# Kernel tuning notes

Measured on AMD Instinct MI355X. Metric: run time of the kernel, lower is better.

The kernel has to match this reference:

```python
import jax, jax.numpy as jnp
import numpy as np
from jax import lax

KSIZE = 7
EPS = 1e-10


def _circular_mask(k=KSIZE):
    # faithful to EdgeLoss.cal_mask: inclusive circle, normalized by count
    xs = np.arange(k, dtype=np.float32)
    d2 = (xs[:, None] + 0.5 - k / 2) ** 2 + (xs[None, :] + 0.5 - k / 2) ** 2
    m = (d2 <= ((k - 1) / 2) ** 2).astype(np.float32)
    return jnp.asarray(m / m.sum())


def _gather_logp(prob, target):
    # prob: (B,C,H,W), target: (B,H,W) int -> log prob at target class, (B,1,H,W)
    logpt = jnp.log(prob + EPS)
    return jnp.take_along_axis(logpt, target[:, None, :, :], axis=1)


def _focal0(prob, target):
    # FocalLoss(gamma=0, alpha=None): mean of -log p_t
    return jnp.mean(-_gather_logp(prob, target))


def _dice(prob, target):
    t = target.astype(prob.dtype)          # (B,H,W)
    p = prob[:, 1, :, :]                   # foreground channel
    I = jnp.sum(p * t, axis=(1, 2))
    U = jnp.sum(p + t, axis=(1, 2))
    return 1.0 - jnp.mean(2.0 * I / (U + EPS))


def _edge(prob, target, mask):
    # circular box-filter average of target == unfold+mask sum (zero padding)
    t = target.astype(prob.dtype)[:, None, :, :]  # (B,1,H,W)
    ave = lax.conv_general_dilated(t, mask[None, None, :, :], (1, 1), 'SAME')
    at = jnp.abs(t - ave)                          # edge weight (B,1,H,W)
    lp = _gather_logp(prob, target)                # (B,1,H,W)
    return jnp.mean(-lp * at)


def _calloss(prob, target, sigmas, mask):
    return (_focal0(prob, target) / sigmas[0]
            + _dice(prob, target) / sigmas[1]
            + _edge(prob, target, mask) / sigmas[2])


def setup_inputs() -> dict:
    key = jax.random.key(0)
    k1, k2, k3, k4, k5 = jax.random.split(key, 5)
    N, M, B, C, H, W = 2, 1, 8, 2, 1024, 1024
    predictions = jax.random.normal(k1, (N, B, C, H, W), dtype=jnp.float32)
    Diss = jax.random.uniform(k2, (M, B, C, H, W), dtype=jnp.float32)
    target = jax.random.randint(k3, (B, H, W), 0, 2, dtype=jnp.int32)
    diff = jax.random.normal(k4, (), dtype=jnp.float32)
    sigma = jax.random.uniform(k5, (3,), dtype=jnp.float32, minval=0.5, maxval=1.5)
    return {"predictions": predictions, "Diss": Diss, "target": target,
            "diff": diff, "sigma": sigma}


def reference(predictions, Diss, target, diff, sigma):
    mask = _circular_mask()
    sigmas = sigma * sigma
    loss = jnp.asarray(0.0, dtype=predictions.dtype)
    for i in range(predictions.shape[0]):            # deep-supervision heads
        prob = jax.nn.softmax(predictions[i], axis=1)
        loss = loss + _calloss(prob, target, sigmas, mask)
    for j in range(Diss.shape[0]):                   # already-probabilities
        loss = loss + _calloss(Diss[j], target, sigmas, mask)
    loss = loss + diff                               # len(diff) != 0 branch
    loss = loss + jnp.sum(jnp.log(sigmas)) / 2
    return loss
```

## Files before the change

### kernel.cpp

```cpp
#include <hip/hip_runtime.h>
#include <math.h>

#define BB 8
#define HH 1024
#define WW 1024
#define HW (1024*1024)

#define TW 128
#define TH 16
#define HALO_H (TH+6)
#define TSTRIDE 136
#define NCOPY 32
#define NSLOT 18

__global__ __launch_bounds__(256, 8)
void loss_main(const float* __restrict__ pred,
               const float* __restrict__ diss,
               const int*   __restrict__ target,
               double*      __restrict__ acc)
{
    __shared__ __align__(16) unsigned char tile[HALO_H][TSTRIDE];
    __shared__ __align__(16) unsigned char h5[HALO_H][TW];
    __shared__ __align__(16) unsigned char h7[HALO_H][TW];
    __shared__ float red[4][12];

    const int bx = blockIdx.x;
    const int by = blockIdx.y;
    const int b  = blockIdx.z;
    const int x0 = bx * TW, y0 = by * TH;
    const int tid = threadIdx.x;
    const int txx = tid & 31;
    const int ty  = tid >> 5;

    const int* tgt_b = target + (size_t)b * HW;
    for (int ch = tid; ch < HALO_H * 34; ch += 256) {
        int r = ch / 34;
        int m = ch - r * 34;
        int gy  = y0 - 3 + r;
        int gxb = x0 - 4 + 4 * m;
        unsigned v = 0u;
        if (gy >= 0 && gy < HH) {
            if (gxb >= 0 && gxb + 3 < WW) {
                const int4 iv = *(const int4*)(tgt_b + (size_t)gy * WW + gxb);
                v = (unsigned)(iv.x & 0xff)
                  | ((unsigned)(iv.y & 0xff) << 8)
                  | ((unsigned)(iv.z & 0xff) << 16)
                  | ((unsigned)(iv.w & 0xff) << 24);
            } else {
                #pragma unroll
                for (int j = 0; j < 4; ++j) {
                    int gx = gxb + j;
                    if (gx >= 0 && gx < WW)
                        v |= (unsigned)(tgt_b[(size_t)gy * WW + gx] & 0xff) << (8 * j);
                }
            }
        }
        *(unsigned*)&tile[r][4 * m] = v;
    }
    __syncthreads();

    for (int g = tid; g < HALO_H * 32; g += 256) {
        int r  = g >> 5;
        int xg = (g & 31) << 2;
        unsigned c0 = *(const unsigned*)&tile[r][xg];
        unsigned c1 = *(const unsigned*)&tile[r][xg + 4];
        unsigned c2 = *(const unsigned*)&tile[r][xg + 8];
        unsigned A1 = (c0 >> 8)  | (c1 << 24);
        unsigned A2 = (c0 >> 16) | (c1 << 16);
        unsigned A3 = (c0 >> 24) | (c1 << 8);
        unsigned A5 = (c1 >> 8)  | (c2 << 24);
        unsigned A6 = (c1 >> 16) | (c2 << 16);
        unsigned A7 = (c1 >> 24) | (c2 << 8);
        unsigned v5 = A2 + A3 + c1 + A5 + A6;
        unsigned v7 = v5 + A1 + A7;
        *(unsigned*)&h5[r][xg] = v5;
        *(unsigned*)&h7[r][xg] = v7;
    }
    __syncthreads();

    const float* p00 = pred + ((size_t)(0 * BB + b) * 2 + 0) * HW;
    const float* p01 = p00 + HW;
    const float* p10 = pred + ((size_t)(1 * BB + b) * 2 + 0) * HW;
    const float* p11 = p10 + HW;
    const float* q0  = diss + ((size_t)b * 2 + 0) * HW;
    const float* q1  = q0 + HW;

    float sf0=0.f, se0=0.f, si0=0.f, su0=0.f;
    float sf1=0.f, se1=0.f, si1=0.f, su1=0.f;
    float sf2=0.f, se2=0.f, si2=0.f, su2=0.f;

    const int x  = txx * 4;
    const int gx = x0 + x;
    #pragma unroll
    for (int k = 0; k < 2; ++k) {
        const int r  = ty + 8 * k;
        const int gy = y0 + r;
        const size_t off = (size_t)gy * WW + gx;

        const unsigned t4   = *(const unsigned*)&tile[r + 3][x + 4];
        const unsigned cnt4 = *(const unsigned*)&tile[r    ][x + 4]
                            + *(const unsigned*)&tile[r + 6][x + 4]
                            + *(const unsigned*)&h5[r + 1][x]
                            + *(const unsigned*)&h5[r + 2][x]
                            + *(const unsigned*)&h7[r + 3][x]
                            + *(const unsigned*)&h5[r + 4][x]
                            + *(const unsigned*)&h5[r + 5][x];

        float4 v00 = *(const float4*)(p00 + off);
        float4 v01 = *(const float4*)(p01 + off);
        float4 v10 = *(const float4*)(p10 + off);
        float4 v11 = *(const float4*)(p11 + off);
        float4 w0  = *(const float4*)(q0  + off);
        float4 w1  = *(const float4*)(q1  + off);

        #pragma unroll
        for (int j = 0; j < 4; ++j) {
            const unsigned tb = (t4 >> (8 * j)) & 0xffu;
            const float t  = (float)tb;
            const float at = fabsf(t - (float)((cnt4 >> (8 * j)) & 0xffu) * (1.0f / 29.0f));
            {
                float a0 = ((const float*)&v00)[j], a1 = ((const float*)&v01)[j];
                float p1v = __builtin_amdgcn_rcpf(1.0f + __expf(a0 - a1));
                float pt  = (tb != 0u) ? p1v : 1.0f - p1v;
                float lp  = __logf(pt + 1e-10f);
                sf0 -= lp; se0 -= lp * at; si0 += p1v * t; su0 += p1v + t;
            }
            {
                float a0 = ((const float*)&v10)[j], a1 = ((const float*)&v11)[j];
                float p1v = __builtin_amdgcn_rcpf(1.0f + __expf(a0 - a1));
                float pt  = (tb != 0u) ? p1v : 1.0f - p1v;
                float lp  = __logf(pt + 1e-10f);
                sf1 -= lp; se1 -= lp * at; si1 += p1v * t; su1 += p1v + t;
            }
            {
                float d0 = ((const float*)&w0)[j], d1 = ((const float*)&w1)[j];
                float pt = (tb != 0u) ? d1 : d0;
                float lp = __logf(pt + 1e-10f);
                sf2 -= lp; se2 -= lp * at; si2 += d1 * t; su2 += d1 + t;
            }
        }
    }

    float vals[12] = {sf0,se0,si0,su0, sf1,se1,si1,su1, sf2,se2,si2,su2};
    #pragma unroll
    for (int j = 0; j < 12; ++j) {
        float v = vals[j];
        #pragma unroll
        for (int s = 32; s > 0; s >>= 1) v += __shfl_down(v, s, 64);
        vals[j] = v;
    }
    const int wave = tid >> 6;
    const int lane = tid & 63;
    if (lane == 0) {
        #pragma unroll
        for (int j = 0; j < 12; ++j) red[wave][j] = vals[j];
    }
    __syncthreads();
    if (tid < 12) {
        double s = (double)red[0][tid] + (double)red[1][tid]
                 + (double)red[2][tid] + (double)red[3][tid];
        const int img  = tid >> 2;
        const int what = tid & 3;
        int slot;
        if      (what == 0) slot = 0;
        else if (what == 1) slot = 1;
        else if (what == 2) slot = 2 + b;
        else                slot = 10 + b;
        const int copy = (by * 8 + bx) & (NCOPY - 1);
        unsafeAtomicAdd(acc + ((size_t)(img * NSLOT + slot) * NCOPY + copy), s);
    }
}

__global__ __launch_bounds__(256)
void finalize_kernel(const double* __restrict__ acc,
                     const float*  __restrict__ diff,
                     const float*  __restrict__ sigma,
                     float*        __restrict__ out)
{
    __shared__ double ssum[54];
    const int t = threadIdx.x;
    if (t < 216) {
        const int slot_lin = t >> 2;
        const int part     = t & 3;
        const double* p = acc + (size_t)slot_lin * NCOPY + part * 8;
        double s = 0.0;
        #pragma unroll
        for (int j = 0; j < 8; ++j) s += p[j];
        s += __shfl_down(s, 1, 64);
        s += __shfl_down(s, 2, 64);
        if (part == 0) ssum[slot_lin] = s;
    }
    __syncthreads();
    if (t == 0) {
        const double sig0 = (double)sigma[0] * (double)sigma[0];
        const double sig1 = (double)sigma[1] * (double)sigma[1];
        const double sig2 = (double)sigma[2] * (double)sigma[2];
        const double inv  = 1.0 / (double)((size_t)BB * HW);
        double loss = 0.0;
        for (int i = 0; i < 3; ++i) {
            const double* A = ssum + i * NSLOT;
            double focal = A[0] * inv;
            double edge  = A[1] * inv;
            double dsum  = 0.0;
            for (int b = 0; b < BB; ++b)
                dsum += 2.0 * A[2 + b] / (A[10 + b] + 1e-10);
            double dice = 1.0 - dsum / (double)BB;
            loss += focal / sig0 + dice / sig1 + edge / sig2;
        }
        loss += (double)diff[0];
        loss += 0.5 * (log(sig0) + log(sig1) + log(sig2));
        out[0] = (float)loss;
    }
}

extern "C" void kernel_launch(void* const* d_in, const int* in_sizes, int n_in,
                              void* d_out, int out_size, void* d_ws, size_t ws_size,
                              hipStream_t stream)
{
    const float* pred   = (const float*)d_in[0];
    const float* diss   = (const float*)d_in[1];
    const int*   target = (const int*)  d_in[2];
    const float* diff   = (const float*)d_in[3];
    const float* sigma  = (const float*)d_in[4];
    double* acc = (double*)d_ws;

    hipMemsetAsync(d_ws, 0, (size_t)3 * NSLOT * NCOPY * sizeof(double), stream);

    dim3 grid(WW / TW, HH / TH, BB);
    loss_main<<<grid, 256, 0, stream>>>(pred, diss, target, acc);
    finalize_kernel<<<1, 256, 0, stream>>>(acc, diff, sigma, (float*)d_out);
}
```

Before: 271.4 us.

## Prefetch prediction loads before target staging and spread atomic accumulator copies

Issues all twelve float4 global loads of predictions and Diss before the target tile is staged into LDS and the box sums are built, so that memory latency overlaps the halo construction and barriers. It hoists the LDS neighbourhood-count reads, accumulates the target sum once instead of once per image, and lowers the occupancy hint to 6 to make room for the extra live registers. It also doubles the number of accumulator copies and changes their layout to copy-major with a stride of 64, which spreads atomic contention across more addresses. The cost is higher register pressure and lower occupancy.

After: 272.0 us. No clear change (+0.2%).

```diff
diff --git a/kernel.cpp b/kernel.cpp
--- a/kernel.cpp
+++ b/kernel.cpp
@@ -10,10 +10,11 @@
 #define TH 16
 #define HALO_H (TH+6)
 #define TSTRIDE 136
-#define NCOPY 32
+#define NCOPY 64
+#define CSTRIDE 64
 #define NSLOT 18
 
-__global__ __launch_bounds__(256, 8)
+__global__ __launch_bounds__(256, 6)
 void loss_main(const float* __restrict__ pred,
                const float* __restrict__ diss,
                const int*   __restrict__ target,
@@ -31,6 +32,31 @@
     const int tid = threadIdx.x;
     const int txx = tid & 31;
     const int ty  = tid >> 5;
+
+    const float* p00 = pred + ((size_t)(0 * BB + b) * 2 + 0) * HW;
+    const float* p01 = p00 + HW;
+    const float* p10 = pred + ((size_t)(1 * BB + b) * 2 + 0) * HW;
+    const float* p11 = p10 + HW;
+    const float* q0  = diss + ((size_t)b * 2 + 0) * HW;
+    const float* q1  = q0 + HW;
+
+    const int x  = txx * 4;
+    const int gx = x0 + x;
+    const size_t offA = (size_t)(y0 + ty) * WW + gx;
+    const size_t offB = offA + (size_t)8 * WW;
+
+    const float4 v00a = *(const float4*)(p00 + offA);
+    const float4 v01a = *(const float4*)(p01 + offA);
+    const float4 v10a = *(const float4*)(p10 + offA);
+    const float4 v11a = *(const float4*)(p11 + offA);
+    const float4 w0a  = *(const float4*)(q0  + offA);
+    const float4 w1a  = *(const float4*)(q1  + offA);
+    const float4 v00b = *(const float4*)(p00 + offB);
+    const float4 v01b = *(const float4*)(p01 + offB);
+    const float4 v10b = *(const float4*)(p10 + offB);
+    const float4 v11b = *(const float4*)(p11 + offB);
+    const float4 w0b  = *(const float4*)(q0  + offB);
+    const float4 w1b  = *(const float4*)(q1  + offB);
 
     const int* tgt_b = target + (size_t)b * HW;
     for (int ch = tid; ch < HALO_H * 34; ch += 256) {
@@ -49,9 +75,9 @@
             } else {
                 #pragma unroll
                 for (int j = 0; j < 4; ++j) {
-                    int gx = gxb + j;
-                    if (gx >= 0 && gx < WW)
-                        v |= (unsigned)(tgt_b[(size_t)gy * WW + gx] & 0xff) << (8 * j);
+                    int gxj = gxb + j;
+                    if (gxj >= 0 && gxj < WW)
+                        v |= (unsigned)(tgt_b[(size_t)gy * WW + gxj] & 0xff) << (8 * j);
                 }
             }
         }
@@ -78,70 +104,69 @@
     }
     __syncthreads();
 
-    const float* p00 = pred + ((size_t)(0 * BB + b) * 2 + 0) * HW;
-    const float* p01 = p00 + HW;
-    const float* p10 = pred + ((size_t)(1 * BB + b) * 2 + 0) * HW;
-    const float* p11 = p10 + HW;
-    const float* q0  = diss + ((size_t)b * 2 + 0) * HW;
-    const float* q1  = q0 + HW;
-
-    float sf0=0.f, se0=0.f, si0=0.f, su0=0.f;
-    float sf1=0.f, se1=0.f, si1=0.f, su1=0.f;
-    float sf2=0.f, se2=0.f, si2=0.f, su2=0.f;
-
-    const int x  = txx * 4;
-    const int gx = x0 + x;
+    float sf0=0.f, se0=0.f, si0=0.f, sp0=0.f;
+    float sf1=0.f, se1=0.f, si1=0.f, sp1=0.f;
+    float sf2=0.f, se2=0.f, si2=0.f, sd1=0.f;
+    float st = 0.f;
+
+    const unsigned t4a   = *(const unsigned*)&tile[ty + 3][x + 4];
+    const unsigned cnt4a = *(const unsigned*)&tile[ty    ][x + 4]
+                         + *(const unsigned*)&tile[ty + 6][x + 4]
+                         + *(const unsigned*)&h5[ty + 1][x]
+                         + *(const unsigned*)&h5[ty + 2][x]
+                         + *(const unsigned*)&h7[ty + 3][x]
+                         + *(const unsigned*)&h5[ty + 4][x]
+                         + *(const unsigned*)&h5[ty + 5][x];
+    const unsigned t4b   = *(const unsigned*)&tile[ty + 11][x + 4];
+    const unsigned cnt4b = *(const unsigned*)&tile[ty +  8][x + 4]
+                         + *(const unsigned*)&tile[ty + 14][x + 4]
+                         + *(const unsigned*)&h5[ty +  9][x]
+                         + *(const unsigned*)&h5[ty + 10][x]
+                         + *(const unsigned*)&h7[ty + 11][x]
+                         + *(const unsigned*)&h5[ty + 12][x]
+                         + *(const unsigned*)&h5[ty + 13][x];
+
     #pragma unroll
     for (int k = 0; k < 2; ++k) {
-        const int r  = ty + 8 * k;
-        const int gy = y0 + r;
-        const size_t off = (size_t)gy * WW + gx;
-
-        const unsigned t4   = *(const unsigned*)&tile[r + 3][x + 4];
-        const unsigned cnt4 = *(const unsigned*)&tile[r    ][x + 4]
-                            + *(const unsigned*)&tile[r + 6][x + 4]
-                            + *(const unsigned*)&h5[r + 1][x]
-                            + *(const unsigned*)&h5[r + 2][x]
-                            + *(const unsigned*)&h7[r + 3][x]
-                            + *(const unsigned*)&h5[r + 4][x]
-                            + *(const unsigned*)&h5[r + 5][x];
-
-        float4 v00 = *(const float4*)(p00 + off);
-        float4 v01 = *(const float4*)(p01 + off);
-        float4 v10 = *(const float4*)(p10 + off);
-        float4 v11 = *(const float4*)(p11 + off);
-        float4 w0  = *(const float4*)(q0  + off);
-        float4 w1  = *(const float4*)(q1  + off);
+        const unsigned t4   = k ? t4b   : t4a;
+        const unsigned cnt4 = k ? cnt4b : cnt4a;
+        const float4&  v00  = k ? v00b : v00a;
+        const float4&  v01  = k ? v01b : v01a;
+        const float4&  v10  = k ? v10b : v10a;
+        const float4&  v11  = k ? v11b : v11a;
+        const float4&  w0   = k ? w0b  : w0a;
+        const float4&  w1   = k ? w1b  : w1a;
 
         #pragma unroll
         for (int j = 0; j < 4; ++j) {
             const unsigned tb = (t4 >> (8 * j)) & 0xffu;
             const float t  = (float)tb;
             const float at = fabsf(t - (float)((cnt4 >> (8 * j)) & 0xffu) * (1.0f / 29.0f));
+            st += t;
             {
                 float a0 = ((const float*)&v00)[j], a1 = ((const float*)&v01)[j];
                 float p1v = __builtin_amdgcn_rcpf(1.0f + __expf(a0 - a1));
                 float pt  = (tb != 0u) ? p1v : 1.0f - p1v;
                 float lp  = __logf(pt + 1e-10f);
-                sf0 -= lp; se0 -= lp * at; si0 += p1v * t; su0 += p1v + t;
+                sf0 -= lp; se0 -= lp * at; si0 += p1v * t; sp0 += p1v;
             }
             {
                 float a0 = ((const float*)&v10)[j], a1 = ((const float*)&v11)[j];
                 float p1v = __builtin_amdgcn_rcpf(1.0f + __expf(a0 - a1));
                 float pt  = (tb != 0u) ? p1v : 1.0f - p1v;
                 float lp  = __logf(pt + 1e-10f);
-                sf1 -= lp; se1 -= lp * at; si1 += p1v * t; su1 += p1v + t;
+                sf1 -= lp; se1 -= lp * at; si1 += p1v * t; sp1 += p1v;
             }
             {
                 float d0 = ((const float*)&w0)[j], d1 = ((const float*)&w1)[j];
                 float pt = (tb != 0u) ? d1 : d0;
                 float lp = __logf(pt + 1e-10f);
-                sf2 -= lp; se2 -= lp * at; si2 += d1 * t; su2 += d1 + t;
+                sf2 -= lp; se2 -= lp * at; si2 += d1 * t; sd1 += d1;
             }
         }
     }
 
-    float vals[12] = {sf0,se0,si0,su0, sf1,se1,si1,su1, sf2,se2,si2,su2};
+    float vals[12] = {sf0,se0,si0,sp0+st, sf1,se1,si1,sp1+st, sf2,se2,si2,sd1+st};
     #pragma unroll
     for (int j = 0; j < 12; ++j) {
         float v = vals[j];
@@ -167,7 +192,7 @@
         else if (what == 2) slot = 2 + b;
         else                slot = 10 + b;
         const int copy = (by * 8 + bx) & (NCOPY - 1);
-        unsafeAtomicAdd(acc + ((size_t)(img * NSLOT + slot) * NCOPY + copy), s);
+        unsafeAtomicAdd(acc + (size_t)copy * CSTRIDE + (img * NSLOT + slot), s);
     }
 }
 
@@ -182,10 +207,10 @@
     if (t < 216) {
         const int slot_lin = t >> 2;
         const int part     = t & 3;
-        const double* p = acc + (size_t)slot_lin * NCOPY + part * 8;
+        const double* p = acc + slot_lin + (size_t)part * 16 * CSTRIDE;
         double s = 0.0;
         #pragma unroll
-        for (int j = 0; j < 8; ++j) s += p[j];
+        for (int j = 0; j < 16; ++j) s += p[(size_t)j * CSTRIDE];
         s += __shfl_down(s, 1, 64);
         s += __shfl_down(s, 2, 64);
         if (part == 0) ssum[slot_lin] = s;
@@ -224,7 +249,7 @@
     const float* sigma  = (const float*)d_in[4];
     double* acc = (double*)d_ws;
 
-    hipMemsetAsync(d_ws, 0, (size_t)3 * NSLOT * NCOPY * sizeof(double), stream);
+    hipMemsetAsync(d_ws, 0, (size_t)NCOPY * CSTRIDE * sizeof(double), stream);
 
     dim3 grid(WW / TW, HH / TH, BB);
     loss_main<<<grid, 256, 0, stream>>>(pred, diss, target, acc);
```

## Pipeline per-block row slabs with async global-to-LDS double buffering

Applied to the files above, without the earlier changes.

Each block now covers a 128x128 region and walks it in 8-row slabs. Prediction and Diss rows are staged into double-buffered LDS with async global_load_lds, and the next target tile and its horizontal sums are prepared while the current slab is computed. This hides memory latency inside each block rather than relying on many short-lived blocks. It also counts target sums once per block instead of per image, and spreads the atomic accumulators over more copies with a transposed layout. The cost is a larger LDS footprint, fewer resident blocks, and more barriers.

Result: slower. 277.8 us (+2.3%).

```diff
diff --git a/kernel.cpp b/kernel.cpp
--- a/kernel.cpp
+++ b/kernel.cpp
@@ -8,157 +8,253 @@
 
 #define TW 128
 #define TH 16
-#define HALO_H (TH+6)
-#define TSTRIDE 136
-#define NCOPY 32
+#define HALO_H 22
+#define TBS 136
+#define NCHUNK (HALO_H*34)
+#define NT 8
+#define NSLAB (NT*2)
+#define NCOPY 64
+#define CSTRIDE 64
 #define NSLOT 18
 
-__global__ __launch_bounds__(256, 8)
+typedef const __attribute__((address_space(1))) unsigned GU;
+typedef __attribute__((address_space(3))) unsigned LU;
+__device__ __forceinline__ void async16(const float* g, const void* lds) {
+    __builtin_amdgcn_global_load_lds((GU*)g, (LU*)lds, 16, 0, 0);
+}
+__device__ __forceinline__ void wait_vm3() {
+    asm volatile("s_waitcnt vmcnt(3)" ::: "memory");
+    __builtin_amdgcn_sched_barrier(0);
+}
+__device__ __forceinline__ void wait_vm0() {
+    asm volatile("s_waitcnt vmcnt(0)" ::: "memory");
+    __builtin_amdgcn_sched_barrier(0);
+}
+__device__ __forceinline__ void lds_barrier() {
+    asm volatile("s_waitcnt lgkmcnt(0)" ::: "memory");
+    __builtin_amdgcn_s_barrier();
+    __builtin_amdgcn_sched_barrier(0);
+}
+__device__ __forceinline__ void plain_barrier() {
+    __builtin_amdgcn_s_barrier();
+    __builtin_amdgcn_sched_barrier(0);
+}
+
+__global__ __launch_bounds__(512, 4)
 void loss_main(const float* __restrict__ pred,
                const float* __restrict__ diss,
                const int*   __restrict__ target,
                double*      __restrict__ acc)
 {
-    __shared__ __align__(16) unsigned char tile[HALO_H][TSTRIDE];
-    __shared__ __align__(16) unsigned char h5[HALO_H][TW];
-    __shared__ __align__(16) unsigned char h7[HALO_H][TW];
-    __shared__ float red[4][12];
-
-    const int bx = blockIdx.x;
-    const int by = blockIdx.y;
-    const int b  = blockIdx.z;
-    const int x0 = bx * TW, y0 = by * TH;
+    __shared__ __align__(16) float pbuf[2][6][8][128];
+    __shared__ __align__(16) unsigned char tb[2][HALO_H][TBS];
+    __shared__ __align__(16) unsigned char h5b[2][20][128];
+    __shared__ __align__(16) unsigned char h7b[2][16][128];
+    __shared__ float red[8][12];
+
+    const int bx  = blockIdx.x;
+    const int bys = blockIdx.y;
+    const int b   = blockIdx.z;
+    const int x0 = bx * TW;
+    const int ys = bys * 128;
     const int tid = threadIdx.x;
-    const int txx = tid & 31;
-    const int ty  = tid >> 5;
+    const int w  = tid >> 6;
+    const int ln = tid & 63;
 
     const int* tgt_b = target + (size_t)b * HW;
-    for (int ch = tid; ch < HALO_H * 34; ch += 256) {
-        int r = ch / 34;
-        int m = ch - r * 34;
-        int gy  = y0 - 3 + r;
-        int gxb = x0 - 4 + 4 * m;
-        unsigned v = 0u;
-        if (gy >= 0 && gy < HH) {
-            if (gxb >= 0 && gxb + 3 < WW) {
-                const int4 iv = *(const int4*)(tgt_b + (size_t)gy * WW + gxb);
-                v = (unsigned)(iv.x & 0xff)
-                  | ((unsigned)(iv.y & 0xff) << 8)
-                  | ((unsigned)(iv.z & 0xff) << 16)
-                  | ((unsigned)(iv.w & 0xff) << 24);
+
+    auto issueP = [&](int sn) {
+        const int Xn  = sn & 1;
+        const int gy0 = ys + (sn >> 1) * 16 + (sn & 1) * 8;
+        #pragma unroll
+        for (int k = 0; k < 3; ++k) {
+            const int c  = w + 8 * k;
+            const int pl = c >> 2, rp = c & 3;
+            const float* base = (pl < 4)
+                ? (pred + (size_t)((pl >> 1) * 16 + b * 2 + (pl & 1)) * HW)
+                : (diss + (size_t)(b * 2 + (pl & 1)) * HW);
+            const int gy = gy0 + 2 * rp + (ln >> 5);
+            const int gx = x0 + (ln & 31) * 4;
+            async16(base + (size_t)gy * WW + gx, &pbuf[Xn][pl][2 * rp][0]);
+        }
+    };
+
+    int4 iv0, iv1;
+    int rr0, mm0, rr1, mm1;
+    bool ok0, ok1, act1;
+    auto issueT = [&](int tn) {
+        const int ty0 = ys + tn * 16 - 3;
+        {
+            const int r = tid / 34, m = tid - r * 34;
+            const int gy = ty0 + r;
+            const int gxb = x0 - 4 + 4 * m;
+            const bool rin = (gy >= 0) && (gy < HH);
+            const bool xin = (gxb >= 0) && (gxb + 3 < WW);
+            rr0 = r; mm0 = m; ok0 = rin && xin;
+            iv0 = *(const int4*)(tgt_b + (size_t)(rin ? gy : 0) * WW + (xin ? gxb : 0));
+        }
+        act1 = (tid + 512) < NCHUNK;
+        {
+            const int ch = act1 ? (tid + 512) : 0;
+            const int r = ch / 34, m = ch - r * 34;
+            const int gy = ty0 + r;
+            const int gxb = x0 - 4 + 4 * m;
+            const bool rin = (gy >= 0) && (gy < HH);
+            const bool xin = (gxb >= 0) && (gxb + 3 < WW);
+            rr1 = r; mm1 = m; ok1 = act1 && rin && xin;
+            if (act1)
+                iv1 = *(const int4*)(tgt_b + (size_t)(rin ? gy : 0) * WW + (xin ? gxb : 0));
+        }
+    };
+    auto packT = [&](int tn) {
+        const int Y = tn & 1;
+        unsigned v0 = ok0 ? ((unsigned)(iv0.x & 0xff)
+                           | ((unsigned)(iv0.y & 0xff) << 8)
+                           | ((unsigned)(iv0.z & 0xff) << 16)
+                           | ((unsigned)(iv0.w & 0xff) << 24)) : 0u;
+        *(unsigned*)&tb[Y][rr0][4 * mm0] = v0;
+        if (act1) {
+            unsigned v1 = ok1 ? ((unsigned)(iv1.x & 0xff)
+                               | ((unsigned)(iv1.y & 0xff) << 8)
+                               | ((unsigned)(iv1.z & 0xff) << 16)
+                               | ((unsigned)(iv1.w & 0xff) << 24)) : 0u;
+            *(unsigned*)&tb[Y][rr1][4 * mm1] = v1;
+        }
+    };
+
+    auto doH = [&](int tn) {
+        const int Y = tn & 1;
+        #pragma unroll
+        for (int i = 0; i < 2; ++i) {
+            const int g = tid + 512 * i;
+            if (g >= HALO_H * 32) break;
+            const int r = g >> 5, xg = (g & 31) << 2;
+            unsigned c0 = *(const unsigned*)&tb[Y][r][xg];
+            unsigned c1 = *(const unsigned*)&tb[Y][r][xg + 4];
+            unsigned c2 = *(const unsigned*)&tb[Y][r][xg + 8];
+            unsigned A1 = (c0 >> 8)  | (c1 << 24);
+            unsigned A2 = (c0 >> 16) | (c1 << 16);
+            unsigned A3 = (c0 >> 24) | (c1 << 8);
+            unsigned A5 = (c1 >> 8)  | (c2 << 24);
+            unsigned A6 = (c1 >> 16) | (c2 << 16);
+            unsigned A7 = (c1 >> 24) | (c2 << 8);
+            unsigned v5 = A2 + A3 + c1 + A5 + A6;
+            unsigned v7 = v5 + A1 + A7;
+            if (r >= 1 && r <= 20) *(unsigned*)&h5b[Y][r - 1][xg] = v5;
+            if (r >= 3 && r <= 18) *(unsigned*)&h7b[Y][r - 3][xg] = v7;
+        }
+    };
+
+    float sf0=0.f, se0=0.f, si0=0.f, sp0=0.f;
+    float sf1=0.f, se1=0.f, si1=0.f, sp1=0.f;
+    float sf2=0.f, se2=0.f, si2=0.f, sd1=0.f;
+    float st = 0.f;
+
+    auto doC = [&](int s) {
+        const int t = s >> 1, p = s & 1, X = t & 1, PB = s & 1;
+        const int tr = p * 8 + w;
+        const int hr = tr + 3;
+        const int wb5 = (2 * ln) & ~3;
+        const int wbt = wb5 + 4;
+        const int sh = (ln & 1) * 16;
+        const unsigned t4w = *(const unsigned*)&tb[X][hr][wbt];
+        const unsigned cw  = *(const unsigned*)&tb[X][tr][wbt]
+                           + *(const unsigned*)&tb[X][tr + 6][wbt]
+                           + *(const unsigned*)&h5b[X][hr - 3][wb5]
+                           + *(const unsigned*)&h5b[X][hr - 2][wb5]
+                           + *(const unsigned*)&h5b[X][hr    ][wb5]
+                           + *(const unsigned*)&h5b[X][hr + 1][wb5]
+                           + *(const unsigned*)&h7b[X][hr - 3][wb5];
+        const float2 f00 = *(const float2*)&pbuf[PB][0][w][2 * ln];
+        const float2 f01 = *(const float2*)&pbuf[PB][1][w][2 * ln];
+        const float2 f10 = *(const float2*)&pbuf[PB][2][w][2 * ln];
+        const float2 f11 = *(const float2*)&pbuf[PB][3][w][2 * ln];
+        const float2 g0  = *(const float2*)&pbuf[PB][4][w][2 * ln];
+        const float2 g1  = *(const float2*)&pbuf[PB][5][w][2 * ln];
+        #pragma unroll
+        for (int j = 0; j < 2; ++j) {
+            const unsigned tv = (t4w >> (sh + 8 * j)) & 0xffu;
+            const float tf = (float)tv;
+            const float at = fabsf(tf - (float)((cw >> (sh + 8 * j)) & 0xffu) * (1.0f / 29.0f));
+            st += tf;
+            {
+                float a0 = ((const float*)&f00)[j], a1 = ((const float*)&f01)[j];
+                float p1v = __builtin_amdgcn_rcpf(1.0f + __expf(a0 - a1));
+                float pt  = (tv != 0u) ? p1v : 1.0f - p1v;
+                float lp  = __logf(pt + 1e-10f);
+                sf0 -= lp; se0 -= lp * at; si0 += p1v * tf; sp0 += p1v;
+            }
+            {
+                float a0 = ((const float*)&f10)[j], a1 = ((const float*)&f11)[j];
+                float p1v = __builtin_amdgcn_rcpf(1.0f + __expf(a0 - a1));
+                float pt  = (tv != 0u) ? p1v : 1.0f - p1v;
+                float lp  = __logf(pt + 1e-10f);
+                sf1 -= lp; se1 -= lp * at; si1 += p1v * tf; sp1 += p1v;
+            }
+            {
+                float d0 = ((const float*)&g0)[j], d1 = ((const float*)&g1)[j];
+                float pt = (tv != 0u) ? d1 : d0;
+                float lp = __logf(pt + 1e-10f);
+                sf2 -= lp; se2 -= lp * at; si2 += d1 * tf; sd1 += d1;
+            }
+        }
+    };
+
+    __builtin_amdgcn_sched_barrier(0);
+    issueT(0);
+    __builtin_amdgcn_sched_barrier(0);
+    issueP(0);
+    __builtin_amdgcn_sched_barrier(0);
+    packT(0);
+    lds_barrier();
+    doH(0);
+
+    for (int s = 0; s < NSLAB; ++s) {
+        plain_barrier();
+        const int t = s >> 1;
+        if ((s & 1) == 0) {
+            if (t + 1 < NT) {
+                __builtin_amdgcn_sched_barrier(0);
+                issueT(t + 1);
+                __builtin_amdgcn_sched_barrier(0);
+                issueP(s + 1);
+                __builtin_amdgcn_sched_barrier(0);
+                packT(t + 1);
+                wait_vm3();
             } else {
-                #pragma unroll
-                for (int j = 0; j < 4; ++j) {
-                    int gx = gxb + j;
-                    if (gx >= 0 && gx < WW)
-                        v |= (unsigned)(tgt_b[(size_t)gy * WW + gx] & 0xff) << (8 * j);
-                }
-            }
-        }
-        *(unsigned*)&tile[r][4 * m] = v;
-    }
-    __syncthreads();
-
-    for (int g = tid; g < HALO_H * 32; g += 256) {
-        int r  = g >> 5;
-        int xg = (g & 31) << 2;
-        unsigned c0 = *(const unsigned*)&tile[r][xg];
-        unsigned c1 = *(const unsigned*)&tile[r][xg + 4];
-        unsigned c2 = *(const unsigned*)&tile[r][xg + 8];
-        unsigned A1 = (c0 >> 8)  | (c1 << 24);
-        unsigned A2 = (c0 >> 16) | (c1 << 16);
-        unsigned A3 = (c0 >> 24) | (c1 << 8);
-        unsigned A5 = (c1 >> 8)  | (c2 << 24);
-        unsigned A6 = (c1 >> 16) | (c2 << 16);
-        unsigned A7 = (c1 >> 24) | (c2 << 8);
-        unsigned v5 = A2 + A3 + c1 + A5 + A6;
-        unsigned v7 = v5 + A1 + A7;
-        *(unsigned*)&h5[r][xg] = v5;
-        *(unsigned*)&h7[r][xg] = v7;
-    }
-    __syncthreads();
-
-    const float* p00 = pred + ((size_t)(0 * BB + b) * 2 + 0) * HW;
-    const float* p01 = p00 + HW;
-    const float* p10 = pred + ((size_t)(1 * BB + b) * 2 + 0) * HW;
-    const float* p11 = p10 + HW;
-    const float* q0  = diss + ((size_t)b * 2 + 0) * HW;
-    const float* q1  = q0 + HW;
-
-    float sf0=0.f, se0=0.f, si0=0.f, su0=0.f;
-    float sf1=0.f, se1=0.f, si1=0.f, su1=0.f;
-    float sf2=0.f, se2=0.f, si2=0.f, su2=0.f;
-
-    const int x  = txx * 4;
-    const int gx = x0 + x;
-    #pragma unroll
-    for (int k = 0; k < 2; ++k) {
-        const int r  = ty + 8 * k;
-        const int gy = y0 + r;
-        const size_t off = (size_t)gy * WW + gx;
-
-        const unsigned t4   = *(const unsigned*)&tile[r + 3][x + 4];
-        const unsigned cnt4 = *(const unsigned*)&tile[r    ][x + 4]
-                            + *(const unsigned*)&tile[r + 6][x + 4]
-                            + *(const unsigned*)&h5[r + 1][x]
-                            + *(const unsigned*)&h5[r + 2][x]
-                            + *(const unsigned*)&h7[r + 3][x]
-                            + *(const unsigned*)&h5[r + 4][x]
-                            + *(const unsigned*)&h5[r + 5][x];
-
-        float4 v00 = *(const float4*)(p00 + off);
-        float4 v01 = *(const float4*)(p01 + off);
-        float4 v10 = *(const float4*)(p10 + off);
-        float4 v11 = *(const float4*)(p11 + off);
-        float4 w0  = *(const float4*)(q0  + off);
-        float4 w1  = *(const float4*)(q1  + off);
-
-        #pragma unroll
-        for (int j = 0; j < 4; ++j) {
-            const unsigned tb = (t4 >> (8 * j)) & 0xffu;
-            const float t  = (float)tb;
-            const float at = fabsf(t - (float)((cnt4 >> (8 * j)) & 0xffu) * (1.0f / 29.0f));
-            {
-                float a0 = ((const float*)&v00)[j], a1 = ((const float*)&v01)[j];
-                float p1v = __builtin_amdgcn_rcpf(1.0f + __expf(a0 - a1));
-                float pt  = (tb != 0u) ? p1v : 1.0f - p1v;
-                float lp  = __logf(pt + 1e-10f);
-                sf0 -= lp; se0 -= lp * at; si0 += p1v * t; su0 += p1v + t;
-            }
-            {
-                float a0 = ((const float*)&v10)[j], a1 = ((const float*)&v11)[j];
-                float p1v = __builtin_amdgcn_rcpf(1.0f + __expf(a0 - a1));
-                float pt  = (tb != 0u) ? p1v : 1.0f - p1v;
-                float lp  = __logf(pt + 1e-10f);
-                sf1 -= lp; se1 -= lp * at; si1 += p1v * t; su1 += p1v + t;
-            }
-            {
-                float d0 = ((const float*)&w0)[j], d1 = ((const float*)&w1)[j];
-                float pt = (tb != 0u) ? d1 : d0;
-                float lp = __logf(pt + 1e-10f);
-                sf2 -= lp; se2 -= lp * at; si2 += d1 * t; su2 += d1 + t;
-            }
-        }
-    }
-
-    float vals[12] = {sf0,se0,si0,su0, sf1,se1,si1,su1, sf2,se2,si2,su2};
+                issueP(s + 1);
+                wait_vm3();
+            }
+        } else {
+            if (s + 1 < NSLAB) {
+                issueP(s + 1);
+                doH(t + 1);
+                wait_vm3();
+            } else {
+                wait_vm0();
+            }
+        }
+        lds_barrier();
+        doC(s);
+    }
+
+    float vals[12] = {sf0,se0,si0,sp0+st, sf1,se1,si1,sp1+st, sf2,se2,si2,sd1+st};
     #pragma unroll
     for (int j = 0; j < 12; ++j) {
         float v = vals[j];
         #pragma unroll
-        for (int s = 32; s > 0; s >>= 1) v += __shfl_down(v, s, 64);
+        for (int sft = 32; sft > 0; sft >>= 1) v += __shfl_down(v, sft, 64);
         vals[j] = v;
     }
-    const int wave = tid >> 6;
-    const int lane = tid & 63;
-    if (lane == 0) {
-        #pragma unroll
-        for (int j = 0; j < 12; ++j) red[wave][j] = vals[j];
+    if (ln == 0) {
+        #pragma unroll
+        for (int j = 0; j < 12; ++j) red[w][j] = vals[j];
     }
     __syncthreads();
     if (tid < 12) {
-        double s = (double)red[0][tid] + (double)red[1][tid]
-                 + (double)red[2][tid] + (double)red[3][tid];
+        double sacc = 0.0;
+        #pragma unroll
+        for (int k = 0; k < 8; ++k) sacc += (double)red[k][tid];
         const int img  = tid >> 2;
         const int what = tid & 3;
         int slot;
@@ -166,8 +262,8 @@
         else if (what == 1) slot = 1;
         else if (what == 2) slot = 2 + b;
         else                slot = 10 + b;
-        const int copy = (by * 8 + bx) & (NCOPY - 1);
-        unsafeAtomicAdd(acc + ((size_t)(img * NSLOT + slot) * NCOPY + copy), s);
+        const int copy = (bys * 8 + bx) & (NCOPY - 1);
+        unsafeAtomicAdd(acc + (size_t)copy * CSTRIDE + (img * NSLOT + slot), sacc);
     }
 }
 
@@ -182,10 +278,10 @@
     if (t < 216) {
         const int slot_lin = t >> 2;
         const int part     = t & 3;
-        const double* p = acc + (size_t)slot_lin * NCOPY + part * 8;
+        const double* p = acc + slot_lin + (size_t)part * 16 * CSTRIDE;
         double s = 0.0;
         #pragma unroll
-        for (int j = 0; j < 8; ++j) s += p[j];
+        for (int j = 0; j < 16; ++j) s += p[(size_t)j * CSTRIDE];
         s += __shfl_down(s, 1, 64);
         s += __shfl_down(s, 2, 64);
         if (part == 0) ssum[slot_lin] = s;
@@ -224,9 +320,9 @@
     const float* sigma  = (const float*)d_in[4];
     double* acc = (double*)d_ws;
 
-    hipMemsetAsync(d_ws, 0, (size_t)3 * NSLOT * NCOPY * sizeof(double), stream);
-
-    dim3 grid(WW / TW, HH / TH, BB);
-    loss_main<<<grid, 256, 0, stream>>>(pred, diss, target, acc);
+    (void)hipMemsetAsync(d_ws, 0, (size_t)NCOPY * CSTRIDE * sizeof(double), stream);
+
+    dim3 grid(WW / TW, HH / 128, BB);
+    loss_main<<<grid, 512, 0, stream>>>(pred, diss, target, acc);
     finalize_kernel<<<1, 256, 0, stream>>>(acc, diff, sigma, (float*)d_out);
 }
```
